# Performance work log

Hardware: AMD Instinct MI355X
Metric: run time of the kernel (lower is better)

The kernel has to match this reference:

```python
import jax, jax.numpy as jnp
import numpy as np

N, C, H = 100000, 128, 8
D = C // H  # 16
E = 1600000
EPS = 1e-5
NEG_SLOPE = 0.2


def layer_norm(x, g, b):
    mu = jnp.mean(x, axis=-1, keepdims=True)
    var = jnp.mean(jnp.square(x - mu), axis=-1, keepdims=True)
    return (x - mu) * jax.lax.rsqrt(var + EPS) * g + b


def setup_inputs() -> dict:
    key = jax.random.key(0)
    ks = jax.random.split(key, 16)
    s = lambda fan: 1.0 / np.sqrt(fan)
    return {
        "x0": jax.random.normal(ks[0], (N, C), jnp.float32),
        "edges": jax.random.randint(ks[1], (2, E), 0, N, jnp.int64) if jax.config.jax_enable_x64 else jax.random.randint(ks[1], (2, E), 0, N, jnp.int32),
        "lin_l_w": jax.random.normal(ks[2], (C, C), jnp.float32) * s(C),
        "lin_r_w": jax.random.normal(ks[3], (C, C), jnp.float32) * s(C),
        "att": jax.random.normal(ks[4], (H, D), jnp.float32) * s(D),
        "gat_bias": jnp.zeros((C,), jnp.float32),
        "W_w": jax.random.normal(ks[5], (C, C), jnp.float32) * s(C),
        "g1": jnp.ones((C,), jnp.float32),
        "b1": jnp.zeros((C,), jnp.float32),
        "mlp_w1": jax.random.normal(ks[6], (2 * C, C), jnp.float32) * s(C),
        "mlp_b1": jnp.zeros((2 * C,), jnp.float32),
        "mlp_w2": jax.random.normal(ks[7], (C, 2 * C), jnp.float32) * s(2 * C),
        "mlp_b2": jnp.zeros((C,), jnp.float32),
        "g2": jnp.ones((C,), jnp.float32),
        "b2": jnp.zeros((C,), jnp.float32),
    }


def gatv2(x, edges, lin_l_w, lin_r_w, att, gat_bias):
    # GATv2Conv (concat=True, negative_slope=0.2, eval mode: no dropout)
    src, dst = edges[0], edges[1]
    x_l = (x @ lin_l_w.T).reshape(N, H, D)  # source transform
    x_r = (x @ lin_r_w.T).reshape(N, H, D)  # target transform
    e = jax.nn.leaky_relu(x_l[src] + x_r[dst], NEG_SLOPE)  # [E,H,D]
    logits = jnp.einsum("ehd,hd->eh", e, att)  # [E,H]
    # segment softmax over incoming edges per target node
    m = jax.ops.segment_max(logits, dst, num_segments=N)  # [N,H]
    m = jnp.where(jnp.isfinite(m), m, 0.0)
    ex = jnp.exp(logits - m[dst])
    denom = jax.ops.segment_sum(ex, dst, num_segments=N)  # [N,H]
    alpha = ex / (denom[dst] + 1e-16)  # [E,H]
    out = jax.ops.segment_sum(alpha[:, :, None] * x_l[src], dst, num_segments=N)
    return out.reshape(N, C) + gat_bias


def reference(x0, edges, lin_l_w, lin_r_w, att, gat_bias, W_w, g1, b1,
              mlp_w1, mlp_b1, mlp_w2, mlp_b2, g2, b2):
    x1 = gatv2(x0, edges, lin_l_w, lin_r_w, att, gat_bias)
    x2 = x1 @ W_w.T + x0
    x3 = layer_norm(x2, g1, b1)
    h = jax.nn.relu(x3 @ mlp_w1.T + mlp_b1)
    x4 = h @ mlp_w2.T + mlp_b2 + x3
    return layer_norm(x4, g2, b2)
```

## Files before the change

### kernel.cpp

```cpp
#include <hip/hip_runtime.h>

#define NN 100000
#define CC 128
#define HHEADS 8
#define EE 1600000
#define NB 196
#define BCAP 10240
#define BSTRIDE 16
#define P1C 3125

typedef unsigned short u16;
typedef unsigned int u32;
typedef __attribute__((ext_vector_type(8))) u16 u16x8;
typedef __attribute__((ext_vector_type(4))) u16 u16x4;
typedef __attribute__((ext_vector_type(8))) __bf16 bf16x8;
typedef __attribute__((ext_vector_type(4))) float f32x4;
typedef __attribute__((ext_vector_type(2))) float f32x2;

__device__ __forceinline__ float bf2f(u16 u) {
    union { u32 i; float f; } v; v.i = ((u32)u) << 16; return v.f;
}
__device__ __forceinline__ u16 f2bf(float f) {
    union { float f; u32 i; } v; v.f = f;
    u32 r = v.i + 0x7FFFu + ((v.i >> 16) & 1u);
    return (u16)(r >> 16);
}
__device__ __forceinline__ float fexp2(float x) {
    float r;
    asm volatile("v_exp_f32 %0, %1" : "=v"(r) : "v"(x));
    return r;
}

__device__ __forceinline__ f32x4 mfma16(u16x8 a, u16x8 b, f32x4 c) {
    return __builtin_amdgcn_mfma_f32_16x16x32_bf16(
        __builtin_bit_cast(bf16x8, a), __builtin_bit_cast(bf16x8, b), c, 0, 0, 0);
}

#define GLOAD(gp, lp) __builtin_amdgcn_global_load_lds( \
    (const __attribute__((address_space(1))) u32*)(gp), \
    (__attribute__((address_space(3))) u32*)(lp), 16, 0, 0)

__global__ __launch_bounds__(256) void k_init(
    const float* __restrict__ x0, u16* __restrict__ x0b,
    const float* __restrict__ s0, const float* __restrict__ s1,
    const float* __restrict__ s2, const float* __restrict__ s3,
    const float* __restrict__ s4,
    u16* __restrict__ d0, u16* __restrict__ d1, u16* __restrict__ d2,
    u16* __restrict__ d3, u16* __restrict__ d4,
    int* __restrict__ bucketCnt)
{
    int b = blockIdx.x, tid = threadIdx.x;
    if (b < 2048) {
        const int n = NN * CC;
        const int stride = 2048 * 256 * 4;
        for (int i = (b * 256 + tid) * 4; i < n; i += stride) {
            float4 v = *(const float4*)(x0 + i);
            u16x4 o;
            o.x = f2bf(v.x); o.y = f2bf(v.y); o.z = f2bf(v.z); o.w = f2bf(v.w);
            *(u16x4*)(x0b + i) = o;
        }
    } else if (b < 2160) {
        int wb = b - 2048;
        const float* s; u16* d; int boff;
        if (wb < 16)      { s = s0; d = d0; boff = wb; }
        else if (wb < 32) { s = s1; d = d1; boff = wb - 16; }
        else if (wb < 48) { s = s2; d = d2; boff = wb - 32; }
        else if (wb < 80) { s = s3; d = d3; boff = wb - 48; }
        else              { s = s4; d = d4; boff = wb - 80; }
        int i = boff * 1024 + tid * 4;
        float4 v = *(const float4*)(s + i);
        u16x4 o;
        o.x = f2bf(v.x); o.y = f2bf(v.y); o.z = f2bf(v.z); o.w = f2bf(v.w);
        *(u16x4*)(d + i) = o;
    } else {
        for (int i = tid; i < NB * BSTRIDE; i += 256) bucketCnt[i] = 0;
    }
}

__global__ __launch_bounds__(256) void k_p1(const int* __restrict__ src,
                                            const int* __restrict__ dst,
                                            int* __restrict__ bucketCnt,
                                            u32* __restrict__ bucketEdges)
{
    __shared__ u32 s_src[P1C];
    __shared__ u32 s_dst[P1C];
    __shared__ u32 hist[256], ssum[256], bstart[256], base[256], seq[256];
    const int b = blockIdx.x, tid = threadIdx.x;
    const int beg = b * P1C;

    hist[tid] = 0; seq[tid] = 0;
    __syncthreads();

    int es[13], ds[13];
#pragma unroll
    for (int j = 0; j < 13; j++) {
        int o = tid + j * 256;
        if (o < P1C) { es[j] = src[beg + o]; ds[j] = dst[beg + o]; }
        else { es[j] = -1; ds[j] = 0; }
    }
#pragma unroll
    for (int j = 0; j < 13; j++)
        if (es[j] >= 0) atomicAdd(&hist[(u32)ds[j] >> 9], 1u);
    __syncthreads();

    u32 h = hist[tid];
    ssum[tid] = h;
    __syncthreads();
    for (int o = 1; o < 256; o <<= 1) {
        u32 v = ssum[tid];
        u32 a = (tid >= o) ? ssum[tid - o] : 0;
        __syncthreads();
        ssum[tid] = v + a;
        __syncthreads();
    }
    bstart[tid] = ssum[tid] - h;
    if (tid < NB) base[tid] = h ? (u32)atomicAdd(&bucketCnt[tid * BSTRIDE], (int)h) : 0u;
    __syncthreads();

#pragma unroll
    for (int j = 0; j < 13; j++) {
        if (es[j] >= 0) {
            u32 bb = (u32)ds[j] >> 9;
            u32 r = atomicAdd(&seq[bb], 1u);
            u32 pos = bstart[bb] + r;
            s_src[pos] = (u32)es[j];
            s_dst[pos] = (u32)ds[j];
        }
    }
    __syncthreads();

    for (int i = tid; i < P1C; i += 256) {
        u32 d = s_dst[i];
        u32 bb = d >> 9;
        u32 go = base[bb] + ((u32)i - bstart[bb]);
        if (go < BCAP)
            bucketEdges[(size_t)bb * BCAP + go] = s_src[i] | ((d & 511u) << 17);
    }
}

__global__ __launch_bounds__(256) void k_p2(const int* __restrict__ bucketCnt,
                                            u32* __restrict__ bucketEdges,
                                            int* __restrict__ offs,
                                            int* __restrict__ cnt)
{
    __shared__ u32 ebuf[BCAP];
    __shared__ u32 ncnt[512], loff[512], ssum[256];
    const int b = blockIdx.x, tid = threadIdx.x;
    int n = bucketCnt[b * BSTRIDE]; n = n < BCAP ? n : BCAP;
    u32* be = bucketEdges + (size_t)b * BCAP;

    for (int i = tid; i < n; i += 256) ebuf[i] = be[i];
    ncnt[tid] = 0; ncnt[tid + 256] = 0;
    __syncthreads();
    for (int i = tid; i < n; i += 256) atomicAdd(&ncnt[(ebuf[i] >> 17) & 511], 1u);
    __syncthreads();

    u32 a0 = ncnt[2 * tid], a1 = ncnt[2 * tid + 1];
    ssum[tid] = a0 + a1;
    __syncthreads();
    for (int o = 1; o < 256; o <<= 1) {
        u32 v = ssum[tid];
        u32 add = (tid >= o) ? ssum[tid - o] : 0;
        __syncthreads();
        ssum[tid] = v + add;
        __syncthreads();
    }
    u32 excl = ssum[tid] - (a0 + a1);
    loff[2 * tid] = excl;
    loff[2 * tid + 1] = excl + a0;

    int node0 = b * 512 + 2 * tid;
    if (node0 < NN)     { offs[node0]     = b * BCAP + (int)excl;            cnt[node0]     = (int)a0; }
    if (node0 + 1 < NN) { offs[node0 + 1] = b * BCAP + (int)(excl + a0);     cnt[node0 + 1] = (int)a1; }

    ncnt[tid] = 0; ncnt[tid + 256] = 0;
    __syncthreads();
    for (int i = tid; i < n; i += 256) {
        u32 e = ebuf[i];
        u32 ln = (e >> 17) & 511;
        u32 r = atomicAdd(&ncnt[ln], 1u);
        be[loff[ln] + r] = e & 0x1FFFFu;
    }
}

template<int K, bool BIAS, bool RELU, bool RESIDB, bool LNF>
__global__ __launch_bounds__(256, 4) void k_gemm(
    const u16* __restrict__ A, const u16* __restrict__ B,
    const float* __restrict__ bias, const u16* __restrict__ residb,
    const float* __restrict__ g, const float* __restrict__ bln,
    float* __restrict__ outf, u16* __restrict__ outb, int M, int NC)
{
    __shared__ __align__(16) u16 As[128 * 64];
    __shared__ __align__(16) u16 Bs[128 * 64];
    __shared__ float lsum[2][128], lsq[2][128];

    const int tid = threadIdx.x;
    const int lane = tid & 63;
    const int w = tid >> 6;
    const int wr = w >> 1, wc = w & 1;
    const int row0 = blockIdx.x * 128;
    const int col0 = blockIdx.y * 128;
    f32x4 acc[4][4] = {};

    for (int kt = 0; kt < K; kt += 64) {
#pragma unroll
        for (int i = 0; i < 4; i++) {
            int c = i * 256 + tid;
            int r = c >> 3;
            int kc = (c & 7) * 8;
            int ar = row0 + r; ar = ar < M ? ar : M - 1;
            GLOAD(A + (size_t)ar * K + kt + kc, As + r * 64 + kc);
            GLOAD(B + (size_t)(col0 + r) * K + kt + kc, Bs + r * 64 + kc);
        }
        asm volatile("s_waitcnt vmcnt(0)" ::: "memory");
        __syncthreads();
#pragma unroll
        for (int kk = 0; kk < 2; kk++) {
            const int ko = kk * 32 + (lane >> 4) * 8;
            u16x8 af[4], bfr[4];
#pragma unroll
            for (int m = 0; m < 4; m++)
                af[m] = *(const u16x8*)(As + (wr * 64 + m * 16 + (lane & 15)) * 64 + ko);
#pragma unroll
            for (int n = 0; n < 4; n++)
                bfr[n] = *(const u16x8*)(Bs + (wc * 64 + n * 16 + (lane & 15)) * 64 + ko);
#pragma unroll
            for (int m = 0; m < 4; m++)
#pragma unroll
                for (int n = 0; n < 4; n++)
                    acc[m][n] = mfma16(af[m], bfr[n], acc[m][n]);
        }
        __syncthreads();
    }

    const int rbase = wr * 64 + ((lane >> 4) << 2);
    const int cbase = wc * 64 + (lane & 15);

    if constexpr (!LNF) {
#pragma unroll
        for (int m = 0; m < 4; m++) {
#pragma unroll
            for (int j = 0; j < 4; j++) {
                int gr = row0 + rbase + m * 16 + j;
                if (gr < M) {
                    size_t rowoff = (size_t)gr * NC;
#pragma unroll
                    for (int n = 0; n < 4; n++) {
                        int gc = col0 + cbase + n * 16;
                        float v = acc[m][n][j];
                        if constexpr (BIAS)  v += bias[gc];
                        if constexpr (RELU)  v = fmaxf(v, 0.f);
                        if (outf) outf[rowoff + gc] = v;
                        if (outb) outb[rowoff + gc] = f2bf(v);
                    }
                }
            }
        }
    } else {
        float gv[4], bv[4];
#pragma unroll
        for (int n = 0; n < 4; n++) { gv[n] = g[cbase + n * 16]; bv[n] = bln[cbase + n * 16]; }
#pragma unroll
        for (int m = 0; m < 4; m++) {
#pragma unroll
            for (int j = 0; j < 4; j++) {
                int lr = rbase + m * 16 + j;
                int gr = row0 + lr; gr = gr < M ? gr : M - 1;
                float s = 0.f, q = 0.f;
#pragma unroll
                for (int n = 0; n < 4; n++) {
                    float v = acc[m][n][j];
                    if constexpr (BIAS)   v += bias[cbase + n * 16];
                    if constexpr (RESIDB) v += bf2f(residb[(size_t)gr * 128 + cbase + n * 16]);
                    if constexpr (RELU)   v = fmaxf(v, 0.f);
                    acc[m][n][j] = v;
                    s += v; q += v * v;
                }
                s += __shfl_xor(s, 1, 16); q += __shfl_xor(q, 1, 16);
                s += __shfl_xor(s, 2, 16); q += __shfl_xor(q, 2, 16);
                s += __shfl_xor(s, 4, 16); q += __shfl_xor(q, 4, 16);
                s += __shfl_xor(s, 8, 16); q += __shfl_xor(q, 8, 16);
                if ((lane & 15) == 0) { lsum[wc][lr] = s; lsq[wc][lr] = q; }
            }
        }
        __syncthreads();
#pragma unroll
        for (int m = 0; m < 4; m++) {
#pragma unroll
            for (int j = 0; j < 4; j++) {
                int lr = rbase + m * 16 + j;
                int gr = row0 + lr;
                if (gr < M) {
                    float s = lsum[0][lr] + lsum[1][lr];
                    float q = lsq[0][lr] + lsq[1][lr];
                    float mu = s * (1.f / 128.f);
                    float var = q * (1.f / 128.f) - mu * mu;
                    float rs = rsqrtf(var + 1e-5f);
                    size_t rowoff = (size_t)gr * 128;
#pragma unroll
                    for (int n = 0; n < 4; n++) {
                        float y = fmaf((acc[m][n][j] - mu) * rs, gv[n], bv[n]);
                        int gc = cbase + n * 16;
                        if (outf) outf[rowoff + gc] = y;
                        if (outb) outb[rowoff + gc] = f2bf(y);
                    }
                }
            }
        }
    }
}

__global__ __launch_bounds__(256) void k_gat(const u16* __restrict__ xlr,
                                             const u32* __restrict__ csr,
                                             const int* __restrict__ offs,
                                             const int* __restrict__ cnt,
                                             const float* __restrict__ att,
                                             const float* __restrict__ gbias,
                                             u16* __restrict__ x1b)
{
    const int node = blockIdx.x * 4 + (threadIdx.x >> 6);
    const int lane = threadIdx.x & 63;
    const int slot = lane >> 4;
    const int sub  = lane & 15;
    const int c0   = sub * 8;
    const float L2E = 1.44269504f;

    f32x4 alo = *(const f32x4*)(att + c0);
    f32x4 ahi = *(const f32x4*)(att + c0 + 4);
    f32x2 av[4];
    av[0] = f32x2{alo[0], alo[1]} * L2E; av[1] = f32x2{alo[2], alo[3]} * L2E;
    av[2] = f32x2{ahi[0], ahi[1]} * L2E; av[3] = f32x2{ahi[2], ahi[3]} * L2E;

    u16x8 xr8 = *(const u16x8*)(xlr + (size_t)node * 256 + 128 + c0);
    f32x2 xrv[4];
#pragma unroll
    for (int j = 0; j < 4; j++) xrv[j] = f32x2{bf2f(xr8[2 * j]), bf2f(xr8[2 * j + 1])};

    const int beg = offs[node];
    const int deg = cnt[node];
    const int ng = (deg + 3) >> 2;

    float s = 0.f;
    f32x2 accv[4] = {};

    u16x8 xgA = {}, xgB = {};
    int ixC = 0;
    if (deg > 0) {
        int dm1 = deg - 1;
        int e0 = slot      < dm1 ? slot      : dm1;
        int e1 = slot + 4  < dm1 ? slot + 4  : dm1;
        int e2 = slot + 8  < dm1 ? slot + 8  : dm1;
        int i0 = (int)csr[beg + e0];
        int i1 = (int)csr[beg + e1];
        ixC    = (int)csr[beg + e2];
        xgA = *(const u16x8*)(xlr + (size_t)i0 * 256 + c0);
        xgB = *(const u16x8*)(xlr + (size_t)i1 * 256 + c0);
    }

    for (int g = 0; g < ng; g++) {
        u16x8 cur = xgA;
        xgA = xgB;
        xgB = *(const u16x8*)(xlr + (size_t)ixC * 256 + c0);
        int en = 4 * (g + 3) + slot; en = en < deg - 1 ? en : deg - 1;
        ixC = (int)csr[beg + (en > 0 ? en : 0)];

        const int e = 4 * g + slot;
        f32x2 xlv[4];
        f32x2 dot = {0.f, 0.f};
#pragma unroll
        for (int j = 0; j < 4; j++) {
            f32x2 xl = f32x2{bf2f(cur[2 * j]), bf2f(cur[2 * j + 1])};
            xlv[j] = xl;
            f32x2 t = xl + xrv[j];
            f32x2 t2 = t * 0.2f;
            f32x2 lr = f32x2{fmaxf(t.x, t2.x), fmaxf(t.y, t2.y)};
            dot += av[j] * lr;
        }
        float p = dot.x + dot.y;
        p += __shfl_xor(p, 1);
        float wgt = (e < deg) ? fexp2(p) : 0.f;
        s += wgt;
#pragma unroll
        for (int j = 0; j < 4; j++) accv[j] += xlv[j] * wgt;
    }

    s += __shfl_xor(s, 16);
    s += __shfl_xor(s, 32);
#pragma unroll
    for (int j = 0; j < 4; j++) {
        accv[j].x += __shfl_xor(accv[j].x, 16);
        accv[j].y += __shfl_xor(accv[j].y, 16);
        accv[j].x += __shfl_xor(accv[j].x, 32);
        accv[j].y += __shfl_xor(accv[j].y, 32);
    }

    if (slot == 0) {
        float inv = 1.f / (s + 1e-16f);
        u16x8 o;
#pragma unroll
        for (int j = 0; j < 4; j++) {
            o[2 * j]     = f2bf(fmaf(accv[j].x, inv, gbias[c0 + 2 * j]));
            o[2 * j + 1] = f2bf(fmaf(accv[j].y, inv, gbias[c0 + 2 * j + 1]));
        }
        *(u16x8*)(x1b + (size_t)node * CC + c0) = o;
    }
}

extern "C" void kernel_launch(void* const* d_in, const int* in_sizes, int n_in,
                              void* d_out, int out_size, void* d_ws, size_t ws_size,
                              hipStream_t stream) {
    const float* x0    = (const float*)d_in[0];
    const int*   edges = (const int*)d_in[1];
    const float* lin_l = (const float*)d_in[2];
    const float* lin_r = (const float*)d_in[3];
    const float* att   = (const float*)d_in[4];
    const float* gbias = (const float*)d_in[5];
    const float* Ww    = (const float*)d_in[6];
    const float* g1    = (const float*)d_in[7];
    const float* b1    = (const float*)d_in[8];
    const float* w1    = (const float*)d_in[9];
    const float* mb1   = (const float*)d_in[10];
    const float* w2    = (const float*)d_in[11];
    const float* mb2   = (const float*)d_in[12];
    const float* g2    = (const float*)d_in[13];
    const float* b2    = (const float*)d_in[14];
    float* out = (float*)d_out;

    char* ws = (char*)d_ws;
    size_t off = 0;
    auto alloc = [&](size_t bytes) {
        char* p = ws + off;
        off += (bytes + 255) & ~(size_t)255;
        return p;
    };
    u16*   x0b   = (u16*)alloc((size_t)NN * CC * 2);
    u16*   xlr   = (u16*)alloc((size_t)NN * 256 * 2);
    u16*   x1b   = (u16*)alloc((size_t)NN * CC * 2);
    u16*   Wa    = (u16*)alloc(256 * 128 * 2);
    u16*   Wb    = (u16*)alloc(128 * 128 * 2);
    u16*   W1    = (u16*)alloc(256 * 128 * 2);
    u16*   W2    = (u16*)alloc(128 * 256 * 2);
    int*   bucketCnt   = (int*)alloc((size_t)NB * BSTRIDE * 4);
    u32*   bucketEdges = (u32*)alloc((size_t)NB * BCAP * 4);
    int*   offsA       = (int*)alloc((size_t)NN * 4);
    int*   cntA        = (int*)alloc((size_t)NN * 4);
    u16*   x3b = x0b;
    u16*   hb  = xlr;
    (void)in_sizes; (void)n_in; (void)out_size; (void)ws_size;

    k_init<<<2161, 256, 0, stream>>>(x0, x0b, lin_l, lin_r, Ww, w1, w2,
                                     Wa, Wa + 16384, Wb, W1, W2, bucketCnt);

    k_p1<<<512, 256, 0, stream>>>(edges, edges + EE, bucketCnt, bucketEdges);
    k_p2<<<NB, 256, 0, stream>>>(bucketCnt, bucketEdges, offsA, cntA);

    k_gemm<128, false, false, false, false><<<dim3(782, 2), 256, 0, stream>>>(
        x0b, Wa, nullptr, nullptr, nullptr, nullptr, nullptr, xlr, NN, 256);

    k_gat<<<NN / 4, 256, 0, stream>>>(xlr, bucketEdges, offsA, cntA, att, gbias, x1b);

    k_gemm<128, false, false, true, true><<<dim3(782, 1), 256, 0, stream>>>(
        x1b, Wb, nullptr, x0b, g1, b1, nullptr, x3b, NN, 128);

    k_gemm<128, true, true, false, false><<<dim3(782, 2), 256, 0, stream>>>(
        x3b, W1, mb1, nullptr, nullptr, nullptr, nullptr, hb, NN, 256);

    k_gemm<256, true, false, true, true><<<dim3(782, 1), 256, 0, stream>>>(
        hb, W2, mb2, x3b, g2, b2, out, nullptr, NN, 128);
}
```

Before: 226.7 us.

## Fuse edge bucketing into init kernel and XOR-swizzle GEMM LDS tiles

After: 222.3 us. 2.0% less time.

```diff
diff --git a/kernel.cpp b/kernel.cpp
--- a/kernel.cpp
+++ b/kernel.cpp
@@ -40,27 +40,82 @@
     (const __attribute__((address_space(1))) u32*)(gp), \
     (__attribute__((address_space(3))) u32*)(lp), 16, 0, 0)
 
-__global__ __launch_bounds__(256) void k_init(
+__global__ __launch_bounds__(256) void k_pre(
+    const int* __restrict__ src, const int* __restrict__ dst,
+    int* __restrict__ bucketCnt, u32* __restrict__ bucketEdges,
     const float* __restrict__ x0, u16* __restrict__ x0b,
     const float* __restrict__ s0, const float* __restrict__ s1,
     const float* __restrict__ s2, const float* __restrict__ s3,
     const float* __restrict__ s4,
     u16* __restrict__ d0, u16* __restrict__ d1, u16* __restrict__ d2,
-    u16* __restrict__ d3, u16* __restrict__ d4,
-    int* __restrict__ bucketCnt)
+    u16* __restrict__ d3, u16* __restrict__ d4)
 {
-    int b = blockIdx.x, tid = threadIdx.x;
-    if (b < 2048) {
+    const int b = blockIdx.x, tid = threadIdx.x;
+    if (b < 512) {
+        __shared__ u32 s_src[P1C];
+        __shared__ u32 s_dst[P1C];
+        __shared__ u32 hist[256], ssum[256], bstart[256], base[256], seq[256];
+        const int beg = b * P1C;
+
+        hist[tid] = 0; seq[tid] = 0;
+        __syncthreads();
+
+        int es[13], ds[13];
+#pragma unroll
+        for (int j = 0; j < 13; j++) {
+            int o = tid + j * 256;
+            if (o < P1C) { es[j] = src[beg + o]; ds[j] = dst[beg + o]; }
+            else { es[j] = -1; ds[j] = 0; }
+        }
+#pragma unroll
+        for (int j = 0; j < 13; j++)
+            if (es[j] >= 0) atomicAdd(&hist[(u32)ds[j] >> 9], 1u);
+        __syncthreads();
+
+        u32 h = hist[tid];
+        ssum[tid] = h;
+        __syncthreads();
+        for (int o = 1; o < 256; o <<= 1) {
+            u32 v = ssum[tid];
+            u32 a = (tid >= o) ? ssum[tid - o] : 0;
+            __syncthreads();
+            ssum[tid] = v + a;
+            __syncthreads();
+        }
+        bstart[tid] = ssum[tid] - h;
+        if (tid < NB) base[tid] = h ? (u32)atomicAdd(&bucketCnt[tid * BSTRIDE], (int)h) : 0u;
+        __syncthreads();
+
+#pragma unroll
+        for (int j = 0; j < 13; j++) {
+            if (es[j] >= 0) {
+                u32 bb = (u32)ds[j] >> 9;
+                u32 r = atomicAdd(&seq[bb], 1u);
+                u32 pos = bstart[bb] + r;
+                s_src[pos] = (u32)es[j];
+                s_dst[pos] = (u32)ds[j];
+            }
+        }
+        __syncthreads();
+
+        for (int i = tid; i < P1C; i += 256) {
+            u32 d = s_dst[i];
+            u32 bb = d >> 9;
+            u32 go = base[bb] + ((u32)i - bstart[bb]);
+            if (go < BCAP)
+                bucketEdges[(size_t)bb * BCAP + go] = s_src[i] | ((d & 511u) << 17);
+        }
+    } else if (b < 2560) {
         const int n = NN * CC;
         const int stride = 2048 * 256 * 4;
-        for (int i = (b * 256 + tid) * 4; i < n; i += stride) {
+        for (int i = ((b - 512) * 256 + tid) * 4; i < n; i += stride) {
             float4 v = *(const float4*)(x0 + i);
             u16x4 o;
             o.x = f2bf(v.x); o.y = f2bf(v.y); o.z = f2bf(v.z); o.w = f2bf(v.w);
             *(u16x4*)(x0b + i) = o;
         }
-    } else if (b < 2160) {
-        int wb = b - 2048;
+    } else {
+        int wb = b - 2560;
         const float* s; u16* d; int boff;
         if (wb < 16)      { s = s0; d = d0; boff = wb; }
         else if (wb < 32) { s = s1; d = d1; boff = wb - 16; }
@@ -72,69 +127,6 @@
         u16x4 o;
         o.x = f2bf(v.x); o.y = f2bf(v.y); o.z = f2bf(v.z); o.w = f2bf(v.w);
         *(u16x4*)(d + i) = o;
-    } else {
-        for (int i = tid; i < NB * BSTRIDE; i += 256) bucketCnt[i] = 0;
-    }
-}
-
-__global__ __launch_bounds__(256) void k_p1(const int* __restrict__ src,
-                                            const int* __restrict__ dst,
-                                            int* __restrict__ bucketCnt,
-                                            u32* __restrict__ bucketEdges)
-{
-    __shared__ u32 s_src[P1C];
-    __shared__ u32 s_dst[P1C];
-    __shared__ u32 hist[256], ssum[256], bstart[256], base[256], seq[256];
-    const int b = blockIdx.x, tid = threadIdx.x;
-    const int beg = b * P1C;
-
-    hist[tid] = 0; seq[tid] = 0;
-    __syncthreads();
-
-    int es[13], ds[13];
-#pragma unroll
-    for (int j = 0; j < 13; j++) {
-        int o = tid + j * 256;
-        if (o < P1C) { es[j] = src[beg + o]; ds[j] = dst[beg + o]; }
-        else { es[j] = -1; ds[j] = 0; }
-    }
-#pragma unroll
-    for (int j = 0; j < 13; j++)
-        if (es[j] >= 0) atomicAdd(&hist[(u32)ds[j] >> 9], 1u);
-    __syncthreads();
-
-    u32 h = hist[tid];
-    ssum[tid] = h;
-    __syncthreads();
-    for (int o = 1; o < 256; o <<= 1) {
-        u32 v = ssum[tid];
-        u32 a = (tid >= o) ? ssum[tid - o] : 0;
-        __syncthreads();
-        ssum[tid] = v + a;
-        __syncthreads();
-    }
-    bstart[tid] = ssum[tid] - h;
-    if (tid < NB) base[tid] = h ? (u32)atomicAdd(&bucketCnt[tid * BSTRIDE], (int)h) : 0u;
-    __syncthreads();
-
-#pragma unroll
-    for (int j = 0; j < 13; j++) {
-        if (es[j] >= 0) {
-            u32 bb = (u32)ds[j] >> 9;
-            u32 r = atomicAdd(&seq[bb], 1u);
-            u32 pos = bstart[bb] + r;
-            s_src[pos] = (u32)es[j];
-            s_dst[pos] = (u32)ds[j];
-        }
-    }
-    __syncthreads();
-
-    for (int i = tid; i < P1C; i += 256) {
-        u32 d = s_dst[i];
-        u32 bb = d >> 9;
-        u32 go = base[bb] + ((u32)i - bstart[bb]);
-        if (go < BCAP)
-            bucketEdges[(size_t)bb * BCAP + go] = s_src[i] | ((d & 511u) << 17);
     }
 }
 
@@ -208,9 +200,10 @@
             int c = i * 256 + tid;
             int r = c >> 3;
             int kc = (c & 7) * 8;
+            int kcs = kc ^ ((r & 7) * 8);
             int ar = row0 + r; ar = ar < M ? ar : M - 1;
-            GLOAD(A + (size_t)ar * K + kt + kc, As + r * 64 + kc);
-            GLOAD(B + (size_t)(col0 + r) * K + kt + kc, Bs + r * 64 + kc);
+            GLOAD(A + (size_t)ar * K + kt + kcs, As + r * 64 + kc);
+            GLOAD(B + (size_t)(col0 + r) * K + kt + kcs, Bs + r * 64 + kc);
         }
         asm volatile("s_waitcnt vmcnt(0)" ::: "memory");
         __syncthreads();
@@ -219,11 +212,15 @@
             const int ko = kk * 32 + (lane >> 4) * 8;
             u16x8 af[4], bfr[4];
 #pragma unroll
-            for (int m = 0; m < 4; m++)
-                af[m] = *(const u16x8*)(As + (wr * 64 + m * 16 + (lane & 15)) * 64 + ko);
-#pragma unroll
-            for (int n = 0; n < 4; n++)
-                bfr[n] = *(const u16x8*)(Bs + (wc * 64 + n * 16 + (lane & 15)) * 64 + ko);
+            for (int m = 0; m < 4; m++) {
+                int rr = wr * 64 + m * 16 + (lane & 15);
+                af[m] = *(const u16x8*)(As + rr * 64 + (ko ^ ((rr & 7) * 8)));
+            }
+#pragma unroll
+            for (int n = 0; n < 4; n++) {
+                int rr = wc * 64 + n * 16 + (lane & 15);
+                bfr[n] = *(const u16x8*)(Bs + rr * 64 + (ko ^ ((rr & 7) * 8)));
+            }
 #pragma unroll
             for (int m = 0; m < 4; m++)
 #pragma unroll
@@ -448,10 +445,11 @@
     u16*   hb  = xlr;
     (void)in_sizes; (void)n_in; (void)out_size; (void)ws_size;
 
-    k_init<<<2161, 256, 0, stream>>>(x0, x0b, lin_l, lin_r, Ww, w1, w2,
-                                     Wa, Wa + 16384, Wb, W1, W2, bucketCnt);
-
-    k_p1<<<512, 256, 0, stream>>>(edges, edges + EE, bucketCnt, bucketEdges);
+    hipMemsetAsync(bucketCnt, 0, (size_t)NB * BSTRIDE * 4, stream);
+    k_pre<<<2672, 256, 0, stream>>>(edges, edges + EE, bucketCnt, bucketEdges,
+                                    x0, x0b, lin_l, lin_r, Ww, w1, w2,
+                                    Wa, Wa + 16384, Wb, W1, W2);
+
     k_p2<<<NB, 256, 0, stream>>>(bucketCnt, bucketEdges, offsA, cntA);
 
     k_gemm<128, false, false, false, false><<<dim3(782, 2), 256, 0, stream>>>(
```
